# Optimization experiments

Hardware: AMD Instinct MI355X
Metric: run time of the kernel (lower is better)

The kernel has to match this reference:

```python
import jax, jax.numpy as jnp
import numpy as np

N, E, F, H, C, K = 50000, 1600000, 256, 6, 16, 40
NEG_SLOPE = 0.2  # PyG GATConv default
EPS = 1e-16


def _gat_layer(x, src, dst, W, a_s, a_d, b, heads, out_ch, concat):
    # linear transform per head: [N, heads, out_ch]
    h = (x @ W).reshape(N, heads, out_ch)
    # per-node attention logits
    al_s = jnp.einsum('nhc,hc->nh', h, a_s)  # source term
    al_d = jnp.einsum('nhc,hc->nh', h, a_d)  # destination term
    # edge-wise score + segment softmax over incoming edges of each dst node
    e = jax.nn.leaky_relu(al_s[src] + al_d[dst], NEG_SLOPE)  # [E', heads]
    m = jax.ops.segment_max(e, dst, num_segments=N)
    ex = jnp.exp(e - m[dst])
    denom = jax.ops.segment_sum(ex, dst, num_segments=N)
    alpha = ex / (denom[dst] + EPS)  # [E', heads]
    # weighted scatter-add aggregation
    out = jax.ops.segment_sum(h[src] * alpha[:, :, None], dst, num_segments=N)
    out = out.reshape(N, heads * out_ch) if concat else out.mean(axis=1)
    return out + b


def setup_inputs() -> dict:
    key = jax.random.key(0)
    ks = jax.random.split(key, 16)
    s = 0.05
    inp = {
        'x': jax.random.normal(ks[0], (N, F), dtype=jnp.float32),
        'edge_index': jax.random.randint(ks[1], (2, E), 0, N, dtype=jnp.int64 if jax.config.jax_enable_x64 else jnp.int32),
        'W1': jax.random.normal(ks[2], (F, H * C), dtype=jnp.float32) * s,
        'a1_s': jax.random.normal(ks[3], (H, C), dtype=jnp.float32) * s,
        'a1_d': jax.random.normal(ks[4], (H, C), dtype=jnp.float32) * s,
        'b1': jnp.zeros((H * C,), dtype=jnp.float32),
        'W2': jax.random.normal(ks[5], (H * C, H * C), dtype=jnp.float32) * s,
        'a2_s': jax.random.normal(ks[6], (H, C), dtype=jnp.float32) * s,
        'a2_d': jax.random.normal(ks[7], (H, C), dtype=jnp.float32) * s,
        'b2': jnp.zeros((H * C,), dtype=jnp.float32),
        'W3': jax.random.normal(ks[8], (H * C, H * C), dtype=jnp.float32) * s,
        'a3_s': jax.random.normal(ks[9], (H, C), dtype=jnp.float32) * s,
        'a3_d': jax.random.normal(ks[10], (H, C), dtype=jnp.float32) * s,
        'b3': jnp.zeros((H * C,), dtype=jnp.float32),
        'W4': jax.random.normal(ks[11], (H * C, K), dtype=jnp.float32) * s,
        'a4_s': jax.random.normal(ks[12], (1, K), dtype=jnp.float32) * s,
        'a4_d': jax.random.normal(ks[13], (1, K), dtype=jnp.float32) * s,
        'b4': jnp.zeros((K,), dtype=jnp.float32),
    }
    return inp


def reference(x, edge_index, W1, a1_s, a1_d, b1, W2, a2_s, a2_d, b2,
              W3, a3_s, a3_d, b3, W4, a4_s, a4_d, b4):
    # PyG GATConv adds self-loops by default
    loops = jnp.arange(N, dtype=edge_index.dtype)
    src = jnp.concatenate([edge_index[0], loops])
    dst = jnp.concatenate([edge_index[1], loops])
    # dropout is identity at eval time
    h = jax.nn.relu(_gat_layer(x, src, dst, W1, a1_s, a1_d, b1, H, C, True))
    h = jax.nn.relu(_gat_layer(h, src, dst, W2, a2_s, a2_d, b2, H, C, True))
    h = jax.nn.relu(_gat_layer(h, src, dst, W3, a3_s, a3_d, b3, H, C, True))
    h = _gat_layer(h, src, dst, W4, a4_s, a4_d, b4, 1, K, False)
    return jax.nn.log_softmax(h, axis=1)
```

## Files before the change

### kernel.cpp

```cpp
#include <hip/hip_runtime.h>
#include <cstdint>
#include <cstddef>

namespace {

constexpr int N  = 50000;
constexpr int E  = 1600000;
constexpr int ET = E + N;
constexpr int F  = 256;
constexpr int H  = 6;
constexpr int C  = 16;
constexpr int HC = H * C;
constexpr int K  = 40;
constexpr int NBUCK = (N + 255) / 256;
constexpr int EPB2  = 8192;
constexpr int HBLK  = (ET + EPB2 - 1) / EPB2;

typedef __attribute__((ext_vector_type(8))) short short8;
typedef __attribute__((ext_vector_type(4))) float f32x4;
typedef __attribute__((ext_vector_type(2))) float f32x2;

__device__ inline uint32_t f2bf(float f) {
  uint32_t u = __float_as_uint(f);
  return (u + 0x7FFFu + ((u >> 16) & 1u)) >> 16;
}
__device__ inline float bflo(uint32_t u) { return __uint_as_float(u << 16); }
__device__ inline float bfhi(uint32_t u) { return __uint_as_float(u & 0xFFFF0000u); }


__global__ void coarse_hist_kernel(const int* __restrict__ ei, int* __restrict__ hist) {
  __shared__ int h[256];
  const int t = threadIdx.x;
  h[t] = 0;
  __syncthreads();
  const int cbase = blockIdx.x * EPB2;
  const int cend = (cbase + EPB2 < ET) ? (cbase + EPB2) : ET;
  for (int e0 = cbase + t * 4; e0 < cend; e0 += 1024) {
    if (e0 + 3 < E && e0 + 3 < cend) {
      int4 dv = *reinterpret_cast<const int4*>(ei + E + e0);
      atomicAdd(&h[dv.x >> 8], 1);
      atomicAdd(&h[dv.y >> 8], 1);
      atomicAdd(&h[dv.z >> 8], 1);
      atomicAdd(&h[dv.w >> 8], 1);
    } else {
#pragma unroll
      for (int q = 0; q < 4; q++) {
        int e = e0 + q;
        if (e < cend) {
          int dd = (e < E) ? ei[E + e] : (e - E);
          atomicAdd(&h[dd >> 8], 1);
        }
      }
    }
  }
  __syncthreads();
  hist[blockIdx.x * 256 + t] = h[t];
}

__global__ void coarse_scan_kernel(const int* __restrict__ hist, int* __restrict__ base,
                                   int* __restrict__ bucket_base, int* __restrict__ rowp) {
  __shared__ int sc[256];
  const int d = threadIdx.x;
  int tot = 0;
#pragma unroll 4
  for (int b = 0; b < HBLK; b++) tot += hist[b * 256 + d];
  sc[d] = tot;
  __syncthreads();
  for (int off = 1; off < 256; off <<= 1) {
    int tv = (d >= off) ? sc[d - off] : 0;
    __syncthreads();
    sc[d] += tv;
    __syncthreads();
  }
  const int excl = sc[d] - tot;
  bucket_base[d] = excl;
  if (d == 255) {
    bucket_base[256] = sc[255];
    rowp[N] = sc[255];
  }
  int run = excl;
#pragma unroll 4
  for (int b = 0; b < HBLK; b++) {
    int v = hist[b * 256 + d];
    base[b * 256 + d] = run;
    run += v;
  }
}

__global__ void coarse_scatter_kernel(const int* __restrict__ ei, const int* __restrict__ base,
                                      uint32_t* __restrict__ keys) {
  __shared__ int cnt[256];
  const int t = threadIdx.x;
  cnt[t] = base[blockIdx.x * 256 + t];
  __syncthreads();
  const int cbase = blockIdx.x * EPB2;
  const int cend = (cbase + EPB2 < ET) ? (cbase + EPB2) : ET;
  for (int e0 = cbase + t * 4; e0 < cend; e0 += 1024) {
    if (e0 + 3 < E && e0 + 3 < cend) {
      int4 dv = *reinterpret_cast<const int4*>(ei + E + e0);
      int4 sv = *reinterpret_cast<const int4*>(ei + e0);
      int p0 = atomicAdd(&cnt[dv.x >> 8], 1);
      keys[p0] = ((uint32_t)dv.x << 16) | (uint32_t)sv.x;
      int p1 = atomicAdd(&cnt[dv.y >> 8], 1);
      keys[p1] = ((uint32_t)dv.y << 16) | (uint32_t)sv.y;
      int p2 = atomicAdd(&cnt[dv.z >> 8], 1);
      keys[p2] = ((uint32_t)dv.z << 16) | (uint32_t)sv.z;
      int p3 = atomicAdd(&cnt[dv.w >> 8], 1);
      keys[p3] = ((uint32_t)dv.w << 16) | (uint32_t)sv.w;
    } else {
#pragma unroll
      for (int q = 0; q < 4; q++) {
        int e = e0 + q;
        if (e < cend) {
          int dd, ssrc;
          if (e < E) { dd = ei[E + e]; ssrc = ei[e]; }
          else       { dd = e - E; ssrc = e - E; }
          int p = atomicAdd(&cnt[dd >> 8], 1);
          keys[p] = ((uint32_t)dd << 16) | (uint32_t)ssrc;
        }
      }
    }
  }
}

__global__ void bucket_sort_kernel(const uint32_t* __restrict__ keys,
                                   const int* __restrict__ bucket_base,
                                   int* __restrict__ rowp, int* __restrict__ col) {
  __shared__ int hist[256];
  __shared__ int sc[256];
  __shared__ int ofs[256];
  const int b = blockIdx.x;
  const int t = threadIdx.x;
  hist[t] = 0;
  __syncthreads();
  const int k0 = bucket_base[b], k1 = bucket_base[b + 1];
  for (int i = k0 + t; i < k1; i += 256)
    atomicAdd(&hist[(keys[i] >> 16) & 255], 1);
  __syncthreads();
  const int v = hist[t];
  sc[t] = v;
  __syncthreads();
  for (int off = 1; off < 256; off <<= 1) {
    int tv = (t >= off) ? sc[t - off] : 0;
    __syncthreads();
    sc[t] += tv;
    __syncthreads();
  }
  ofs[t] = k0 + sc[t] - v;
  const int node = b * 256 + t;
  if (node < N) rowp[node] = ofs[t];
  hist[t] = 0;
  __syncthreads();
  for (int i = k0 + t; i < k1; i += 256) {
    uint32_t key = keys[i];
    int loc = (key >> 16) & 255;
    int p = ofs[loc] + atomicAdd(&hist[loc], 1);
    col[p] = (int)(key & 0xFFFFu);
  }
}


__global__ void deg_hist_kernel(const int* __restrict__ rowp, int* __restrict__ dh) {
  __shared__ int h[256];
  const int t = threadIdx.x;
  h[t] = 0;
  __syncthreads();
  int i = blockIdx.x * 256 + t;
  if (i < N) {
    int deg = rowp[i + 1] - rowp[i];
    if (deg > 255) deg = 255;
    atomicAdd(&h[deg], 1);
  }
  __syncthreads();
  dh[blockIdx.x * 256 + t] = h[t];
}

__global__ void deg_scan_kernel(const int* __restrict__ dh, int* __restrict__ dbase) {
  __shared__ int sc[256];
  const int d = threadIdx.x;
  int tot = 0;
#pragma unroll 4
  for (int b = 0; b < NBUCK; b++) tot += dh[b * 256 + d];
  sc[d] = tot;
  __syncthreads();
  for (int off = 1; off < 256; off <<= 1) {
    int tv = (d >= off) ? sc[d - off] : 0;
    __syncthreads();
    sc[d] += tv;
    __syncthreads();
  }
  int run = sc[d] - tot;
#pragma unroll 4
  for (int b = 0; b < NBUCK; b++) {
    int v = dh[b * 256 + d];
    dbase[b * 256 + d] = run;
    run += v;
  }
}

__global__ void deg_scatter_kernel(const int* __restrict__ rowp, const int* __restrict__ dbase,
                                   int* __restrict__ perm) {
  __shared__ int cnt[256];
  const int t = threadIdx.x;
  cnt[t] = dbase[blockIdx.x * 256 + t];
  __syncthreads();
  int i = blockIdx.x * 256 + t;
  if (i < N) {
    int deg = rowp[i + 1] - rowp[i];
    if (deg > 255) deg = 255;
    int p = atomicAdd(&cnt[deg], 1);
    perm[p] = i;
  }
}


__global__ void tobf16_kernel(const float* __restrict__ src, uint32_t* __restrict__ dst,
                              int n2) {
  int i = blockIdx.x * blockDim.x + threadIdx.x;
  if (i >= n2) return;
  float2 v = reinterpret_cast<const float2*>(src)[i];
  dst[i] = (f2bf(v.y) << 16) | f2bf(v.x);
}


__global__ void cvtW_kernel(const float* __restrict__ W1, const float* __restrict__ W2,
                            const float* __restrict__ W3, const float* __restrict__ W4,
                            uint16_t* __restrict__ WT1, uint16_t* __restrict__ WT2,
                            uint16_t* __restrict__ WT3, uint16_t* __restrict__ WT4) {
  constexpr int T1 = 96 * 256, T2 = 96 * 96, T3 = 96 * 96, T4 = 48 * 96;
  int t = blockIdx.x * blockDim.x + threadIdx.x;
  if (t < T1) {
    int n = t / 256, k = t % 256;
    WT1[t] = (uint16_t)f2bf(W1[(size_t)k * 96 + n]);
  } else if (t < T1 + T2) {
    int u = t - T1; int n = u / 96, k = u % 96;
    WT2[u] = (uint16_t)f2bf(W2[(size_t)k * 96 + n]);
  } else if (t < T1 + T2 + T3) {
    int u = t - T1 - T2; int n = u / 96, k = u % 96;
    WT3[u] = (uint16_t)f2bf(W3[(size_t)k * 96 + n]);
  } else if (t < T1 + T2 + T3 + T4) {
    int u = t - T1 - T2 - T3; int n = u / 96, k = u % 96;
    WT4[u] = (n < K) ? (uint16_t)f2bf(W4[(size_t)k * K + n]) : (uint16_t)0;
  }
}


template <int KD>
__launch_bounds__(256)
__global__ void gemm_pack_kernel(const uint32_t* __restrict__ A,
                                 const uint16_t* __restrict__ WT,
                                 const float* __restrict__ as_,
                                 const float* __restrict__ ad_,
                                 uint32_t* __restrict__ recs,
                                 float* __restrict__ aldP) {
  constexpr int KU = KD / 2;
  __shared__ float lds[64][97];
  const int wave = threadIdx.x >> 6;
  const int lane = threadIdx.x & 63;
  const int r = lane & 15, g = lane >> 4;
  const int m0 = (blockIdx.x * 4 + wave) * 16;
  int rowA = m0 + r;
  if (rowA > N - 1) rowA = N - 1;
  const uint32_t* arow = A + (size_t)rowA * KU + g * 4;
  const uint32_t* wt32 = reinterpret_cast<const uint32_t*>(WT);

  f32x4 acc[6];
#pragma unroll
  for (int nt = 0; nt < 6; nt++) acc[nt] = (f32x4){0.f, 0.f, 0.f, 0.f};

#pragma unroll
  for (int ks = 0; ks < KD / 32; ks++) {
    short8 av = *reinterpret_cast<const short8*>(arow + ks * 16);
#pragma unroll
    for (int nt = 0; nt < 6; nt++) {
      short8 bv = *reinterpret_cast<const short8*>(
          wt32 + (size_t)(nt * 16 + r) * KU + ks * 16 + g * 4);
      acc[nt] = __builtin_amdgcn_mfma_f32_16x16x32_bf16(av, bv, acc[nt], 0, 0, 0);
    }
  }

  const int lr0 = wave * 16 + g * 4;
#pragma unroll
  for (int nt = 0; nt < 6; nt++) {
#pragma unroll
    for (int t = 0; t < 4; t++) lds[lr0 + t][nt * 16 + r] = acc[nt][t];
  }
  __syncthreads();

  const int row = threadIdx.x >> 2;
  const int q = threadIdx.x & 3;
  const int grow = blockIdx.x * 64 + row;
  if (grow < N) {
    const float* lr = lds[row];
    uint32_t* rp = recs + (size_t)grow * 32;
#pragma unroll
    for (int w = 0; w < 6; w++) {
      const int c0 = q * 24 + w * 4;
      uint32_t wv = 0;
      wv = (uint32_t)__builtin_amdgcn_cvt_pk_fp8_f32(lr[c0], lr[c0 + 1], (int)wv, false);
      wv = (uint32_t)__builtin_amdgcn_cvt_pk_fp8_f32(lr[c0 + 2], lr[c0 + 3], (int)wv, true);
      rp[q * 6 + w] = wv;
    }
#pragma unroll
    for (int i = 0; i < 3; i++) {
      const int d = q * 3 + i;
      const int hh = d >> 1;
      const float* av = (d & 1) ? ad_ : as_;
      float s = 0.f;
#pragma unroll
      for (int c = 0; c < 16; c++) s += lr[hh * 16 + c] * av[hh * 16 + c];
      if (d & 1) aldP[(size_t)grow * 8 + hh] = s;
      else       rp[24 + hh] = __float_as_uint(s);
    }
  }
}


template <int KD, int NT, int NCOLS, int OST>
__launch_bounds__(256)
__global__ void mfma_gemm_kernel(const uint32_t* __restrict__ A,
                                 const uint16_t* __restrict__ WT,
                                 uint16_t* __restrict__ hOut, int M) {
  constexpr int KU = KD / 2;
  const int wave = threadIdx.x >> 6;
  const int lane = threadIdx.x & 63;
  const int m0 = (blockIdx.x * 4 + wave) * 16;
  if (m0 >= M) return;
  const int r = lane & 15, g = lane >> 4;
  int rowA = m0 + r;
  if (rowA > M - 1) rowA = M - 1;
  const uint32_t* arow = A + (size_t)rowA * KU + g * 4;
  const uint32_t* wt32 = reinterpret_cast<const uint32_t*>(WT);

  f32x4 acc[NT];
#pragma unroll
  for (int nt = 0; nt < NT; nt++) acc[nt] = (f32x4){0.f, 0.f, 0.f, 0.f};

#pragma unroll
  for (int ks = 0; ks < KD / 32; ks++) {
    short8 av = *reinterpret_cast<const short8*>(arow + ks * 16);
#pragma unroll
    for (int nt = 0; nt < NT; nt++) {
      short8 bv = *reinterpret_cast<const short8*>(
          wt32 + (size_t)(nt * 16 + r) * KU + ks * 16 + g * 4);
      acc[nt] = __builtin_amdgcn_mfma_f32_16x16x32_bf16(av, bv, acc[nt], 0, 0, 0);
    }
  }

  const int orow = m0 + g * 4;
#pragma unroll
  for (int nt = 0; nt < NT; nt++) {
    const int ocol = nt * 16 + r;
#pragma unroll
    for (int t = 0; t < 4; t++) {
      int rr = orow + t;
      if (rr < M && ocol < NCOLS)
        hOut[(size_t)rr * OST + ocol] = (uint16_t)f2bf(acc[nt][t]);
    }
  }
}


__global__ void pack4_kernel(const uint32_t* __restrict__ h4B,
                             const float* __restrict__ as_, const float* __restrict__ ad_,
                             uint32_t* __restrict__ recs4, float* __restrict__ ald4) {
  int n = blockIdx.x * 256 + threadIdx.x;
  if (n >= N) return;
  const uint32_t* hp = h4B + (size_t)n * 32;
  float f[40];
  float ss = 0.f, dd = 0.f;
#pragma unroll
  for (int i = 0; i < 20; i++) {
    uint32_t u = hp[i];
    f[2 * i] = bflo(u);
    f[2 * i + 1] = bfhi(u);
  }
#pragma unroll
  for (int c = 0; c < 40; c++) {
    ss += f[c] * as_[c];
    dd += f[c] * ad_[c];
  }
  uint32_t* rp = recs4 + (size_t)n * 16;
#pragma unroll
  for (int q = 0; q < 10; q++) {
    uint32_t w = 0;
    w = (uint32_t)__builtin_amdgcn_cvt_pk_fp8_f32(f[4 * q + 0], f[4 * q + 1], (int)w, false);
    w = (uint32_t)__builtin_amdgcn_cvt_pk_fp8_f32(f[4 * q + 2], f[4 * q + 3], (int)w, true);
    rp[q] = w;
  }
  rp[10] = __float_as_uint(ss);
  ald4[n] = dd;
}


template <int LPN, int NPW, int REC32, int ALSW, int HDIV, int PAD, bool LSM>
__launch_bounds__(256)
__global__ void flash_agg5_kernel(const uint32_t* __restrict__ recs,
                                  const int* __restrict__ rowp,
                                  const int* __restrict__ col,
                                  const int* __restrict__ perm,
                                  const float* __restrict__ aldP,
                                  const float* __restrict__ bias,
                                  uint4* __restrict__ outB4,
                                  float* __restrict__ outF32) {
  const int lane = threadIdx.x & 63;
  const int wave = threadIdx.x >> 6;
  int g = lane / LPN;
  const int li = lane - g * LPN;
  if (g > NPW - 1) g = NPW - 1;
  int idx = (blockIdx.x * 4 + wave) * NPW + g;
  if (idx > N - 1) idx = N - 1;
  const int n = perm[idx];
  const int hh = li / HDIV;
  const float aldv = aldP[(size_t)n * PAD + hh];
  const int b0 = rowp[n];
  const int deg = rowp[n + 1] - b0;
  const int d1 = deg >> 1;
  const int d2 = deg - d1;

  int km = d2;
#pragma unroll
  for (int off = 32; off > 0; off >>= 1) {
    int o = __shfl_xor(km, off);
    km = (o > km) ? o : km;
  }

  float a0 = 0.f, a1 = 0.f, a2 = 0.f, a3 = 0.f;
  float a4 = 0.f, a5 = 0.f, a6 = 0.f, a7 = 0.f;
  float b0f = 0.f, b1f = 0.f, b2f = 0.f, b3f = 0.f;
  float b4f = 0.f, b5f = 0.f, b6f = 0.f, b7f = 0.f;
  float ssA = 0.f, ssB = 0.f;

#pragma unroll 2
  for (int k = 0; k < km; k++) {
    const bool vA = (k < d1);
    const bool vB = (k < d2);
    const int jA = b0 + (vA ? k : 0);
    const int jB = b0 + d1 + (vB ? k : 0);
    const int srcA = col[jA];
    const int srcB = col[jB];
    const uint32_t* recA = recs + (size_t)srcA * REC32;
    const uint32_t* recB = recs + (size_t)srcB * REC32;
    uint2 uA = *reinterpret_cast<const uint2*>(recA + 2 * li);
    uint2 uB = *reinterpret_cast<const uint2*>(recB + 2 * li);
    float lA = __uint_as_float(recA[ALSW + hh]);
    float lB = __uint_as_float(recB[ALSW + hh]);
    float eA = lA + aldv; eA = fmaxf(eA, 0.2f * eA);
    float eB = lB + aldv; eB = fmaxf(eB, 0.2f * eB);
    float pA = __expf(eA); pA = vA ? pA : 0.f;
    float pB = __expf(eB); pB = vB ? pB : 0.f;
    f32x2 cA0 = __builtin_amdgcn_cvt_pk_f32_fp8((int)uA.x, false);
    f32x2 cA1 = __builtin_amdgcn_cvt_pk_f32_fp8((int)uA.x, true);
    f32x2 cA2 = __builtin_amdgcn_cvt_pk_f32_fp8((int)uA.y, false);
    f32x2 cA3 = __builtin_amdgcn_cvt_pk_f32_fp8((int)uA.y, true);
    f32x2 cB0 = __builtin_amdgcn_cvt_pk_f32_fp8((int)uB.x, false);
    f32x2 cB1 = __builtin_amdgcn_cvt_pk_f32_fp8((int)uB.x, true);
    f32x2 cB2 = __builtin_amdgcn_cvt_pk_f32_fp8((int)uB.y, false);
    f32x2 cB3 = __builtin_amdgcn_cvt_pk_f32_fp8((int)uB.y, true);
    a0 += pA * cA0.x; a1 += pA * cA0.y;
    a2 += pA * cA1.x; a3 += pA * cA1.y;
    a4 += pA * cA2.x; a5 += pA * cA2.y;
    a6 += pA * cA3.x; a7 += pA * cA3.y;
    ssA += pA;
    b0f += pB * cB0.x; b1f += pB * cB0.y;
    b2f += pB * cB1.x; b3f += pB * cB1.y;
    b4f += pB * cB2.x; b5f += pB * cB2.y;
    b6f += pB * cB3.x; b7f += pB * cB3.y;
    ssB += pB;
  }

  a0 += b0f; a1 += b1f; a2 += b2f; a3 += b3f;
  a4 += b4f; a5 += b5f; a6 += b6f; a7 += b7f;
  float inv = 1.f / (ssA + ssB + 1e-16f);

  if (!LSM) {
    float o0 = fmaxf(a0 * inv + bias[8 * li + 0], 0.f);
    float o1 = fmaxf(a1 * inv + bias[8 * li + 1], 0.f);
    float o2 = fmaxf(a2 * inv + bias[8 * li + 2], 0.f);
    float o3 = fmaxf(a3 * inv + bias[8 * li + 3], 0.f);
    float o4 = fmaxf(a4 * inv + bias[8 * li + 4], 0.f);
    float o5 = fmaxf(a5 * inv + bias[8 * li + 5], 0.f);
    float o6 = fmaxf(a6 * inv + bias[8 * li + 6], 0.f);
    float o7 = fmaxf(a7 * inv + bias[8 * li + 7], 0.f);
    uint4 w;
    w.x = (f2bf(o1) << 16) | f2bf(o0);
    w.y = (f2bf(o3) << 16) | f2bf(o2);
    w.z = (f2bf(o5) << 16) | f2bf(o4);
    w.w = (f2bf(o7) << 16) | f2bf(o6);
    outB4[(size_t)n * LPN + li] = w;
  } else {
    bool vl = (li < 5);
    float v0 = vl ? a0 * inv + bias[8 * li + 0] : -1e30f;
    float v1 = vl ? a1 * inv + bias[8 * li + 1] : -1e30f;
    float v2 = vl ? a2 * inv + bias[8 * li + 2] : -1e30f;
    float v3 = vl ? a3 * inv + bias[8 * li + 3] : -1e30f;
    float v4 = vl ? a4 * inv + bias[8 * li + 4] : -1e30f;
    float v5 = vl ? a5 * inv + bias[8 * li + 5] : -1e30f;
    float v6 = vl ? a6 * inv + bias[8 * li + 6] : -1e30f;
    float v7 = vl ? a7 * inv + bias[8 * li + 7] : -1e30f;
    float mx = fmaxf(fmaxf(fmaxf(v0, v1), fmaxf(v2, v3)),
                     fmaxf(fmaxf(v4, v5), fmaxf(v6, v7)));
#pragma unroll
    for (int off = 1; off < 8; off <<= 1) mx = fmaxf(mx, __shfl_xor(mx, off));
    float es = 0.f;
    if (vl)
      es = __expf(v0 - mx) + __expf(v1 - mx) + __expf(v2 - mx) + __expf(v3 - mx) +
           __expf(v4 - mx) + __expf(v5 - mx) + __expf(v6 - mx) + __expf(v7 - mx);
#pragma unroll
    for (int off = 1; off < 8; off <<= 1) es += __shfl_xor(es, off);
    float lse = mx + __logf(es);
    if (vl) {
      float* op = outF32 + (size_t)n * K + li * 8;
      float4 w0 = make_float4(v0 - lse, v1 - lse, v2 - lse, v3 - lse);
      float4 w1 = make_float4(v4 - lse, v5 - lse, v6 - lse, v7 - lse);
      *reinterpret_cast<float4*>(op) = w0;
      *reinterpret_cast<float4*>(op + 4) = w1;
    }
  }
}

inline int cdiv(int a, int b) { return (a + b - 1) / b; }

}

extern "C" void kernel_launch(void* const* d_in, const int* in_sizes, int n_in,
                              void* d_out, int out_size, void* d_ws, size_t ws_size,
                              hipStream_t stream) {
  (void)in_sizes; (void)n_in; (void)out_size; (void)ws_size;
  const float* x   = (const float*)d_in[0];
  const int*   ei  = (const int*)d_in[1];
  const float* W1  = (const float*)d_in[2];
  const float* a1s = (const float*)d_in[3];
  const float* a1d = (const float*)d_in[4];
  const float* b1  = (const float*)d_in[5];
  const float* W2  = (const float*)d_in[6];
  const float* a2s = (const float*)d_in[7];
  const float* a2d = (const float*)d_in[8];
  const float* b2  = (const float*)d_in[9];
  const float* W3  = (const float*)d_in[10];
  const float* a3s = (const float*)d_in[11];
  const float* a3d = (const float*)d_in[12];
  const float* b3  = (const float*)d_in[13];
  const float* W4  = (const float*)d_in[14];
  const float* a4s = (const float*)d_in[15];
  const float* a4d = (const float*)d_in[16];
  const float* b4  = (const float*)d_in[17];
  float* out = (float*)d_out;

  char* ws = (char*)d_ws;
  size_t off = 0;
  auto alloc = [&](size_t bytes) {
    void* p = ws + off;
    off = (off + bytes + 255) & ~(size_t)255;
    return p;
  };
  int*      hist  = (int*)alloc((size_t)HBLK * 256 * 4);
  int*      basep = (int*)alloc((size_t)HBLK * 256 * 4);
  int*      bbase = (int*)alloc((size_t)257 * 4);
  int*      rowp  = (int*)alloc((size_t)(N + 1) * 4);
  uint32_t* keys  = (uint32_t*)alloc((size_t)ET * 4);
  int*      col   = (int*)alloc((size_t)ET * 4);
  int*      perm  = (int*)alloc((size_t)N * 4);
  uint32_t* xB    = (uint32_t*)alloc((size_t)N * (F / 2) * 4);
  uint16_t* WT1   = (uint16_t*)alloc((size_t)96 * 256 * 2);
  uint16_t* WT2   = (uint16_t*)alloc((size_t)96 * 96 * 2);
  uint16_t* WT3   = (uint16_t*)alloc((size_t)96 * 96 * 2);
  uint16_t* WT4   = (uint16_t*)alloc((size_t)48 * 96 * 2);
  uint32_t* actB  = (uint32_t*)alloc((size_t)N * (HC / 2) * 4);
  uint32_t* h4B   = (uint32_t*)alloc((size_t)N * 32 * 4);
  uint32_t* recs  = (uint32_t*)alloc((size_t)N * 32 * 4);
  uint32_t* recs4 = (uint32_t*)alloc((size_t)N * 16 * 4);
  float*    aldP  = (float*)alloc((size_t)N * 8 * 4);

  coarse_hist_kernel<<<HBLK, 256, 0, stream>>>(ei, hist);
  coarse_scan_kernel<<<1, 256, 0, stream>>>(hist, basep, bbase, rowp);
  coarse_scatter_kernel<<<HBLK, 256, 0, stream>>>(ei, basep, keys);
  bucket_sort_kernel<<<NBUCK, 256, 0, stream>>>(keys, bbase, rowp, col);

  deg_hist_kernel<<<NBUCK, 256, 0, stream>>>(rowp, hist);
  deg_scan_kernel<<<1, 256, 0, stream>>>(hist, basep);
  deg_scatter_kernel<<<NBUCK, 256, 0, stream>>>(rowp, basep, perm);

  tobf16_kernel<<<cdiv(N * (F / 2), 256), 256, 0, stream>>>(x, xB, N * (F / 2));
  cvtW_kernel<<<cdiv(96 * 256 + 96 * 96 * 2 + 48 * 96, 256), 256, 0, stream>>>(
      W1, W2, W3, W4, WT1, WT2, WT3, WT4);

  const int gN1  = cdiv(N, 256);
  const int gG   = cdiv(N, 64);
  const int gA96 = cdiv(N, 20);
  const int gA40 = cdiv(N, 32);

  gemm_pack_kernel<F><<<gG, 256, 0, stream>>>(xB, WT1, a1s, a1d, recs, aldP);
  flash_agg5_kernel<12, 5, 32, 24, 2, 8, false><<<gA96, 256, 0, stream>>>(
      recs, rowp, col, perm, aldP, b1, (uint4*)actB, nullptr);

  gemm_pack_kernel<HC><<<gG, 256, 0, stream>>>(actB, WT2, a2s, a2d, recs, aldP);
  flash_agg5_kernel<12, 5, 32, 24, 2, 8, false><<<gA96, 256, 0, stream>>>(
      recs, rowp, col, perm, aldP, b2, (uint4*)actB, nullptr);

  gemm_pack_kernel<HC><<<gG, 256, 0, stream>>>(actB, WT3, a3s, a3d, recs, aldP);
  flash_agg5_kernel<12, 5, 32, 24, 2, 8, false><<<gA96, 256, 0, stream>>>(
      recs, rowp, col, perm, aldP, b3, (uint4*)actB, nullptr);

  mfma_gemm_kernel<HC, 3, K, 64><<<gG, 256, 0, stream>>>(actB, WT4, (uint16_t*)h4B, N);
  pack4_kernel<<<gN1, 256, 0, stream>>>(h4B, a4s, a4d, recs4, aldP);
  flash_agg5_kernel<8, 8, 16, 10, 16, 1, true><<<gA40, 256, 0, stream>>>(
      recs4, rowp, col, perm, aldP, b4, nullptr, out);
}
```

Before: 309.3 us.

## Map one lane per head in hidden-layer aggregation, 10 nodes per wave

Hidden-layer aggregation now assigns 6 lanes per destination node, one per head, each loading 16 fp8 features with a uint4 instead of 12 lanes each loading 8. A wave now handles 10 nodes instead of 5, which halves the grid and lowers redundant col/logit loads per edge. The price is more accumulator registers per lane and 4 idle lanes per wave. Separately, the x and weight bf16 conversion kernels are merged into one launch, and the layer-4 log-softmax path becomes its own kernel.

```diff
diff --git a/kernel.cpp b/kernel.cpp
--- a/kernel.cpp
+++ b/kernel.cpp
@@ -214,21 +214,22 @@
 }
 
 
-__global__ void tobf16_kernel(const float* __restrict__ src, uint32_t* __restrict__ dst,
-                              int n2) {
-  int i = blockIdx.x * blockDim.x + threadIdx.x;
-  if (i >= n2) return;
-  float2 v = reinterpret_cast<const float2*>(src)[i];
-  dst[i] = (f2bf(v.y) << 16) | f2bf(v.x);
-}
-
-
-__global__ void cvtW_kernel(const float* __restrict__ W1, const float* __restrict__ W2,
+constexpr int TOB_N2 = N * (F / 2);
+constexpr int T1 = 96 * 256, T2 = 96 * 96, T3 = 96 * 96, T4 = 48 * 96;
+constexpr int CVT_T = T1 + T2 + T3 + T4;
+
+__global__ void prep_kernel(const float* __restrict__ x, uint32_t* __restrict__ xB,
+                            const float* __restrict__ W1, const float* __restrict__ W2,
                             const float* __restrict__ W3, const float* __restrict__ W4,
                             uint16_t* __restrict__ WT1, uint16_t* __restrict__ WT2,
                             uint16_t* __restrict__ WT3, uint16_t* __restrict__ WT4) {
-  constexpr int T1 = 96 * 256, T2 = 96 * 96, T3 = 96 * 96, T4 = 48 * 96;
-  int t = blockIdx.x * blockDim.x + threadIdx.x;
+  int t = blockIdx.x * 256 + threadIdx.x;
+  if (t < TOB_N2) {
+    float2 v = reinterpret_cast<const float2*>(x)[t];
+    xB[t] = (f2bf(v.y) << 16) | f2bf(v.x);
+    return;
+  }
+  t -= TOB_N2;
   if (t < T1) {
     int n = t / 256, k = t % 256;
     WT1[t] = (uint16_t)f2bf(W1[(size_t)k * 96 + n]);
@@ -238,7 +239,7 @@
   } else if (t < T1 + T2 + T3) {
     int u = t - T1 - T2; int n = u / 96, k = u % 96;
     WT3[u] = (uint16_t)f2bf(W3[(size_t)k * 96 + n]);
-  } else if (t < T1 + T2 + T3 + T4) {
+  } else if (t < CVT_T) {
     int u = t - T1 - T2 - T3; int n = u / 96, k = u % 96;
     WT4[u] = (n < K) ? (uint16_t)f2bf(W4[(size_t)k * K + n]) : (uint16_t)0;
   }
@@ -393,26 +394,24 @@
 }
 
 
-template <int LPN, int NPW, int REC32, int ALSW, int HDIV, int PAD, bool LSM>
 __launch_bounds__(256)
-__global__ void flash_agg5_kernel(const uint32_t* __restrict__ recs,
+__global__ void flash_agg6_kernel(const uint32_t* __restrict__ recs,
                                   const int* __restrict__ rowp,
                                   const int* __restrict__ col,
                                   const int* __restrict__ perm,
                                   const float* __restrict__ aldP,
                                   const float* __restrict__ bias,
-                                  uint4* __restrict__ outB4,
-                                  float* __restrict__ outF32) {
+                                  uint4* __restrict__ outB4) {
   const int lane = threadIdx.x & 63;
   const int wave = threadIdx.x >> 6;
-  int g = lane / LPN;
-  const int li = lane - g * LPN;
-  if (g > NPW - 1) g = NPW - 1;
-  int idx = (blockIdx.x * 4 + wave) * NPW + g;
+  int g = lane / 6;
+  if (g > 9) g = 9;
+  int li = lane - g * 6;
+  if (li > 5) li = 5;
+  int idx = (blockIdx.x * 4 + wave) * 10 + g;
   if (idx > N - 1) idx = N - 1;
   const int n = perm[idx];
-  const int hh = li / HDIV;
-  const float aldv = aldP[(size_t)n * PAD + hh];
+  const float aldv = aldP[(size_t)n * 8 + li];
   const int b0 = rowp[n];
   const int deg = rowp[n + 1] - b0;
   const int d1 = deg >> 1;
@@ -425,10 +424,9 @@
     km = (o > km) ? o : km;
   }
 
-  float a0 = 0.f, a1 = 0.f, a2 = 0.f, a3 = 0.f;
-  float a4 = 0.f, a5 = 0.f, a6 = 0.f, a7 = 0.f;
-  float b0f = 0.f, b1f = 0.f, b2f = 0.f, b3f = 0.f;
-  float b4f = 0.f, b5f = 0.f, b6f = 0.f, b7f = 0.f;
+  float accA[16], accB[16];
+#pragma unroll
+  for (int c = 0; c < 16; c++) { accA[c] = 0.f; accB[c] = 0.f; }
   float ssA = 0.f, ssB = 0.f;
 
 #pragma unroll 2
@@ -439,12 +437,93 @@
     const int jB = b0 + d1 + (vB ? k : 0);
     const int srcA = col[jA];
     const int srcB = col[jB];
-    const uint32_t* recA = recs + (size_t)srcA * REC32;
-    const uint32_t* recB = recs + (size_t)srcB * REC32;
+    const uint32_t* recA = recs + (size_t)srcA * 32;
+    const uint32_t* recB = recs + (size_t)srcB * 32;
+    uint4 uA = *reinterpret_cast<const uint4*>(recA + 4 * li);
+    uint4 uB = *reinterpret_cast<const uint4*>(recB + 4 * li);
+    float lA = __uint_as_float(recA[24 + li]);
+    float lB = __uint_as_float(recB[24 + li]);
+    float eA = lA + aldv; eA = fmaxf(eA, 0.2f * eA);
+    float eB = lB + aldv; eB = fmaxf(eB, 0.2f * eB);
+    float pA = __expf(eA); pA = vA ? pA : 0.f;
+    float pB = __expf(eB); pB = vB ? pB : 0.f;
+    const uint32_t wa[4] = {uA.x, uA.y, uA.z, uA.w};
+    const uint32_t wb[4] = {uB.x, uB.y, uB.z, uB.w};
+#pragma unroll
+    for (int w = 0; w < 4; w++) {
+      f32x2 c0 = __builtin_amdgcn_cvt_pk_f32_fp8((int)wa[w], false);
+      f32x2 c1 = __builtin_amdgcn_cvt_pk_f32_fp8((int)wa[w], true);
+      accA[4 * w + 0] += pA * c0.x; accA[4 * w + 1] += pA * c0.y;
+      accA[4 * w + 2] += pA * c1.x; accA[4 * w + 3] += pA * c1.y;
+      f32x2 d0 = __builtin_amdgcn_cvt_pk_f32_fp8((int)wb[w], false);
+      f32x2 dd1 = __builtin_amdgcn_cvt_pk_f32_fp8((int)wb[w], true);
+      accB[4 * w + 0] += pB * d0.x; accB[4 * w + 1] += pB * d0.y;
+      accB[4 * w + 2] += pB * dd1.x; accB[4 * w + 3] += pB * dd1.y;
+    }
+    ssA += pA; ssB += pB;
+  }
+
+  const float inv = 1.f / (ssA + ssB + 1e-16f);
+  uint32_t wout[8];
+#pragma unroll
+  for (int j = 0; j < 8; j++) {
+    float o0 = fmaxf((accA[2 * j] + accB[2 * j]) * inv + bias[16 * li + 2 * j], 0.f);
+    float o1 = fmaxf((accA[2 * j + 1] + accB[2 * j + 1]) * inv + bias[16 * li + 2 * j + 1], 0.f);
+    wout[j] = (f2bf(o1) << 16) | f2bf(o0);
+  }
+  outB4[(size_t)n * 12 + 2 * li]     = make_uint4(wout[0], wout[1], wout[2], wout[3]);
+  outB4[(size_t)n * 12 + 2 * li + 1] = make_uint4(wout[4], wout[5], wout[6], wout[7]);
+}
+
+
+__launch_bounds__(256)
+__global__ void flash_agg_lsm_kernel(const uint32_t* __restrict__ recs,
+                                     const int* __restrict__ rowp,
+                                     const int* __restrict__ col,
+                                     const int* __restrict__ perm,
+                                     const float* __restrict__ aldP,
+                                     const float* __restrict__ bias,
+                                     float* __restrict__ outF32) {
+  const int lane = threadIdx.x & 63;
+  const int wave = threadIdx.x >> 6;
+  const int g = lane >> 3;
+  const int li = lane & 7;
+  int idx = (blockIdx.x * 4 + wave) * 8 + g;
+  if (idx > N - 1) idx = N - 1;
+  const int n = perm[idx];
+  const float aldv = aldP[n];
+  const int b0 = rowp[n];
+  const int deg = rowp[n + 1] - b0;
+  const int d1 = deg >> 1;
+  const int d2 = deg - d1;
+
+  int km = d2;
+#pragma unroll
+  for (int off = 32; off > 0; off >>= 1) {
+    int o = __shfl_xor(km, off);
+    km = (o > km) ? o : km;
+  }
+
+  float a0 = 0.f, a1 = 0.f, a2 = 0.f, a3 = 0.f;
+  float a4 = 0.f, a5 = 0.f, a6 = 0.f, a7 = 0.f;
+  float b0f = 0.f, b1f = 0.f, b2f = 0.f, b3f = 0.f;
+  float b4f = 0.f, b5f = 0.f, b6f = 0.f, b7f = 0.f;
+  float ssA = 0.f, ssB = 0.f;
+
+#pragma unroll 2
+  for (int k = 0; k < km; k++) {
+    const bool vA = (k < d1);
+    const bool vB = (k < d2);
+    const int jA = b0 + (vA ? k : 0);
+    const int jB = b0 + d1 + (vB ? k : 0);
+    const int srcA = col[jA];
+    const int srcB = col[jB];
+    const uint32_t* recA = recs + (size_t)srcA * 16;
+    const uint32_t* recB = recs + (size_t)srcB * 16;
     uint2 uA = *reinterpret_cast<const uint2*>(recA + 2 * li);
     uint2 uB = *reinterpret_cast<const uint2*>(recB + 2 * li);
-    float lA = __uint_as_float(recA[ALSW + hh]);
-    float lB = __uint_as_float(recB[ALSW + hh]);
+    float lA = __uint_as_float(recA[10]);
+    float lB = __uint_as_float(recB[10]);
     float eA = lA + aldv; eA = fmaxf(eA, 0.2f * eA);
     float eB = lB + aldv; eB = fmaxf(eB, 0.2f * eB);
     float pA = __expf(eA); pA = vA ? pA : 0.f;
@@ -473,49 +552,30 @@
   a4 += b4f; a5 += b5f; a6 += b6f; a7 += b7f;
   float inv = 1.f / (ssA + ssB + 1e-16f);
 
-  if (!LSM) {
-    float o0 = fmaxf(a0 * inv + bias[8 * li + 0], 0.f);
-    float o1 = fmaxf(a1 * inv + bias[8 * li + 1], 0.f);
-    float o2 = fmaxf(a2 * inv + bias[8 * li + 2], 0.f);
-    float o3 = fmaxf(a3 * inv + bias[8 * li + 3], 0.f);
-    float o4 = fmaxf(a4 * inv + bias[8 * li + 4], 0.f);
-    float o5 = fmaxf(a5 * inv + bias[8 * li + 5], 0.f);
-    float o6 = fmaxf(a6 * inv + bias[8 * li + 6], 0.f);
-    float o7 = fmaxf(a7 * inv + bias[8 * li + 7], 0.f);
-    uint4 w;
-    w.x = (f2bf(o1) << 16) | f2bf(o0);
-    w.y = (f2bf(o3) << 16) | f2bf(o2);
-    w.z = (f2bf(o5) << 16) | f2bf(o4);
-    w.w = (f2bf(o7) << 16) | f2bf(o6);
-    outB4[(size_t)n * LPN + li] = w;
-  } else {
-    bool vl = (li < 5);
-    float v0 = vl ? a0 * inv + bias[8 * li + 0] : -1e30f;
-    float v1 = vl ? a1 * inv + bias[8 * li + 1] : -1e30f;
-    float v2 = vl ? a2 * inv + bias[8 * li + 2] : -1e30f;
-    float v3 = vl ? a3 * inv + bias[8 * li + 3] : -1e30f;
-    float v4 = vl ? a4 * inv + bias[8 * li + 4] : -1e30f;
-    float v5 = vl ? a5 * inv + bias[8 * li + 5] : -1e30f;
-    float v6 = vl ? a6 * inv + bias[8 * li + 6] : -1e30f;
-    float v7 = vl ? a7 * inv + bias[8 * li + 7] : -1e30f;
-    float mx = fmaxf(fmaxf(fmaxf(v0, v1), fmaxf(v2, v3)),
-                     fmaxf(fmaxf(v4, v5), fmaxf(v6, v7)));
-#pragma unroll
-    for (int off = 1; off < 8; off <<= 1) mx = fmaxf(mx, __shfl_xor(mx, off));
-    float es = 0.f;
-    if (vl)
-      es = __expf(v0 - mx) + __expf(v1 - mx) + __expf(v2 - mx) + __expf(v3 - mx) +
-           __expf(v4 - mx) + __expf(v5 - mx) + __expf(v6 - mx) + __expf(v7 - mx);
-#pragma unroll
-    for (int off = 1; off < 8; off <<= 1) es += __shfl_xor(es, off);
-    float lse = mx + __logf(es);
-    if (vl) {
-      float* op = outF32 + (size_t)n * K + li * 8;
-      float4 w0 = make_float4(v0 - lse, v1 - lse, v2 - lse, v3 - lse);
-      float4 w1 = make_float4(v4 - lse, v5 - lse, v6 - lse, v7 - lse);
-      *reinterpret_cast<float4*>(op) = w0;
-      *reinterpret_cast<float4*>(op + 4) = w1;
-    }
+  bool vl = (li < 5);
+  float v0 = vl ? a0 * inv + bias[8 * li + 0] : -1e30f;
+  float v1 = vl ? a1 * inv + bias[8 * li + 1] : -1e30f;
+  float v2 = vl ? a2 * inv + bias[8 * li + 2] : -1e30f;
+  float v3 = vl ? a3 * inv + bias[8 * li + 3] : -1e30f;
+  float v4 = vl ? a4 * inv + bias[8 * li + 4] : -1e30f;
+  float v5 = vl ? a5 * inv + bias[8 * li + 5] : -1e30f;
+  float v6 = vl ? a6 * inv + bias[8 * li + 6] : -1e30f;
+  float v7 = vl ? a7 * inv + bias[8 * li + 7] : -1e30f;
+  float mx = fmaxf(fmaxf(fmaxf(v0, v1), fmaxf(v2, v3)),
+                   fmaxf(fmaxf(v4, v5), fmaxf(v6, v7)));
+#pragma unroll
+  for (int off = 1; off < 8; off <<= 1) mx = fmaxf(mx, __shfl_xor(mx, off));
+  float es = 0.f;
+  if (vl)
+    es = __expf(v0 - mx) + __expf(v1 - mx) + __expf(v2 - mx) + __expf(v3 - mx) +
+         __expf(v4 - mx) + __expf(v5 - mx) + __expf(v6 - mx) + __expf(v7 - mx);
+#pragma unroll
+  for (int off = 1; off < 8; off <<= 1) es += __shfl_xor(es, off);
+  float lse = mx + __logf(es);
+  if (vl) {
+    float* op = outF32 + (size_t)n * K + li * 8;
+    *reinterpret_cast<float4*>(op) = make_float4(v0 - lse, v1 - lse, v2 - lse, v3 - lse);
+    *reinterpret_cast<float4*>(op + 4) = make_float4(v4 - lse, v5 - lse, v6 - lse, v7 - lse);
   }
 }
 
@@ -581,29 +641,24 @@
   deg_scan_kernel<<<1, 256, 0, stream>>>(hist, basep);
   deg_scatter_kernel<<<NBUCK, 256, 0, stream>>>(rowp, basep, perm);
 
-  tobf16_kernel<<<cdiv(N * (F / 2), 256), 256, 0, stream>>>(x, xB, N * (F / 2));
-  cvtW_kernel<<<cdiv(96 * 256 + 96 * 96 * 2 + 48 * 96, 256), 256, 0, stream>>>(
-      W1, W2, W3, W4, WT1, WT2, WT3, WT4);
+  prep_kernel<<<cdiv(TOB_N2 + CVT_T, 256), 256, 0, stream>>>(
+      x, xB, W1, W2, W3, W4, WT1, WT2, WT3, WT4);
 
   const int gN1  = cdiv(N, 256);
   const int gG   = cdiv(N, 64);
-  const int gA96 = cdiv(N, 20);
+  const int gA96 = cdiv(N, 40);
   const int gA40 = cdiv(N, 32);
 
   gemm_pack_kernel<F><<<gG, 256, 0, stream>>>(xB, WT1, a1s, a1d, recs, aldP);
-  flash_agg5_kernel<12, 5, 32, 24, 2, 8, false><<<gA96, 256, 0, stream>>>(
-      recs, rowp, col, perm, aldP, b1, (uint4*)actB, nullptr);
+  flash_agg6_kernel<<<gA96, 256, 0, stream>>>(recs, rowp, col, perm, aldP, b1, (uint4*)actB);
 
   gemm_pack_kernel<HC><<<gG, 256, 0, stream>>>(actB, WT2, a2s, a2d, recs, aldP);
-  flash_agg5_kernel<12, 5, 32, 24, 2, 8, false><<<gA96, 256, 0, stream>>>(
-      recs, rowp, col, perm, aldP, b2, (uint4*)actB, nullptr);
+  flash_agg6_kernel<<<gA96, 256, 0, stream>>>(recs, rowp, col, perm, aldP, b2, (uint4*)actB);
 
   gemm_pack_kernel<HC><<<gG, 256, 0, stream>>>(actB, WT3, a3s, a3d, recs, aldP);
-  flash_agg5_kernel<12, 5, 32, 24, 2, 8, false><<<gA96, 256, 0, stream>>>(
-      recs, rowp, col, perm, aldP, b3, (uint4*)actB, nullptr);
+  flash_agg6_kernel<<<gA96, 256, 0, stream>>>(recs, rowp, col, perm, aldP, b3, (uint4*)actB);
 
   mfma_gemm_kernel<HC, 3, K, 64><<<gG, 256, 0, stream>>>(actB, WT4, (uint16_t*)h4B, N);
   pack4_kernel<<<gN1, 256, 0, stream>>>(h4B, a4s, a4d, recs4, aldP);
-  flash_agg5_kernel<8, 8, 16, 10, 16, 1, true><<<gA40, 256, 0, stream>>>(
-      recs4, rowp, col, perm, aldP, b4, nullptr, out);
-}
+  flash_agg_lsm_kernel<<<gA40, 256, 0, stream>>>(recs4, rowp, col, perm, aldP, b4, out);
+}
```

Result: slower. 317.6 us (+2.7%).

## Fuse input/weight conversion, fuse layer-4 GEMM with packing, reverse degree order

Applied to the files above, without the earlier changes.

Merges the x-to-bf16 conversion and weight transpose kernels into a single prep kernel. Fuses the final-layer MFMA GEMM with the fp8 record packing and attention logit computation through LDS, removing the intermediate bf16 h4 buffer and one launch. Reverses the degree-sorted node permutation so high-degree nodes are scheduled first, aiming to reduce tail imbalance in aggregation. The fused pack step runs on only one wave per block, which serializes some per-row work.

```diff
diff --git a/kernel.cpp b/kernel.cpp
--- a/kernel.cpp
+++ b/kernel.cpp
@@ -209,26 +209,27 @@
     int deg = rowp[i + 1] - rowp[i];
     if (deg > 255) deg = 255;
     int p = atomicAdd(&cnt[deg], 1);
-    perm[p] = i;
-  }
-}
-
-
-__global__ void tobf16_kernel(const float* __restrict__ src, uint32_t* __restrict__ dst,
-                              int n2) {
-  int i = blockIdx.x * blockDim.x + threadIdx.x;
-  if (i >= n2) return;
-  float2 v = reinterpret_cast<const float2*>(src)[i];
-  dst[i] = (f2bf(v.y) << 16) | f2bf(v.x);
-}
-
-
-__global__ void cvtW_kernel(const float* __restrict__ W1, const float* __restrict__ W2,
+    perm[N - 1 - p] = i;
+  }
+}
+
+
+constexpr int TOB_N2 = N * (F / 2);
+constexpr int T1 = 96 * 256, T2 = 96 * 96, T3 = 96 * 96, T4 = 48 * 96;
+constexpr int CVT_T = T1 + T2 + T3 + T4;
+
+__global__ void prep_kernel(const float* __restrict__ x, uint32_t* __restrict__ xB,
+                            const float* __restrict__ W1, const float* __restrict__ W2,
                             const float* __restrict__ W3, const float* __restrict__ W4,
                             uint16_t* __restrict__ WT1, uint16_t* __restrict__ WT2,
                             uint16_t* __restrict__ WT3, uint16_t* __restrict__ WT4) {
-  constexpr int T1 = 96 * 256, T2 = 96 * 96, T3 = 96 * 96, T4 = 48 * 96;
-  int t = blockIdx.x * blockDim.x + threadIdx.x;
+  int t = blockIdx.x * 256 + threadIdx.x;
+  if (t < TOB_N2) {
+    float2 v = reinterpret_cast<const float2*>(x)[t];
+    xB[t] = (f2bf(v.y) << 16) | f2bf(v.x);
+    return;
+  }
+  t -= TOB_N2;
   if (t < T1) {
     int n = t / 256, k = t % 256;
     WT1[t] = (uint16_t)f2bf(W1[(size_t)k * 96 + n]);
@@ -238,7 +239,7 @@
   } else if (t < T1 + T2 + T3) {
     int u = t - T1 - T2; int n = u / 96, k = u % 96;
     WT3[u] = (uint16_t)f2bf(W3[(size_t)k * 96 + n]);
-  } else if (t < T1 + T2 + T3 + T4) {
+  } else if (t < CVT_T) {
     int u = t - T1 - T2 - T3; int n = u / 96, k = u % 96;
     WT4[u] = (n < K) ? (uint16_t)f2bf(W4[(size_t)k * K + n]) : (uint16_t)0;
   }
@@ -316,80 +317,70 @@
 }
 
 
-template <int KD, int NT, int NCOLS, int OST>
 __launch_bounds__(256)
-__global__ void mfma_gemm_kernel(const uint32_t* __restrict__ A,
-                                 const uint16_t* __restrict__ WT,
-                                 uint16_t* __restrict__ hOut, int M) {
-  constexpr int KU = KD / 2;
+__global__ void gemm_pack4_kernel(const uint32_t* __restrict__ A,
+                                  const uint16_t* __restrict__ WT,
+                                  const float* __restrict__ as_,
+                                  const float* __restrict__ ad_,
+                                  uint32_t* __restrict__ recs4,
+                                  float* __restrict__ ald4) {
+  constexpr int KU = 48;
+  __shared__ float lds[64][49];
   const int wave = threadIdx.x >> 6;
   const int lane = threadIdx.x & 63;
+  const int r = lane & 15, g = lane >> 4;
   const int m0 = (blockIdx.x * 4 + wave) * 16;
-  if (m0 >= M) return;
-  const int r = lane & 15, g = lane >> 4;
   int rowA = m0 + r;
-  if (rowA > M - 1) rowA = M - 1;
+  if (rowA > N - 1) rowA = N - 1;
   const uint32_t* arow = A + (size_t)rowA * KU + g * 4;
   const uint32_t* wt32 = reinterpret_cast<const uint32_t*>(WT);
 
-  f32x4 acc[NT];
-#pragma unroll
-  for (int nt = 0; nt < NT; nt++) acc[nt] = (f32x4){0.f, 0.f, 0.f, 0.f};
-
-#pragma unroll
-  for (int ks = 0; ks < KD / 32; ks++) {
+  f32x4 acc[3];
+#pragma unroll
+  for (int nt = 0; nt < 3; nt++) acc[nt] = (f32x4){0.f, 0.f, 0.f, 0.f};
+
+#pragma unroll
+  for (int ks = 0; ks < 3; ks++) {
     short8 av = *reinterpret_cast<const short8*>(arow + ks * 16);
 #pragma unroll
-    for (int nt = 0; nt < NT; nt++) {
+    for (int nt = 0; nt < 3; nt++) {
       short8 bv = *reinterpret_cast<const short8*>(
           wt32 + (size_t)(nt * 16 + r) * KU + ks * 16 + g * 4);
       acc[nt] = __builtin_amdgcn_mfma_f32_16x16x32_bf16(av, bv, acc[nt], 0, 0, 0);
     }
   }
 
-  const int orow = m0 + g * 4;
-#pragma unroll
-  for (int nt = 0; nt < NT; nt++) {
-    const int ocol = nt * 16 + r;
-#pragma unroll
-    for (int t = 0; t < 4; t++) {
-      int rr = orow + t;
-      if (rr < M && ocol < NCOLS)
-        hOut[(size_t)rr * OST + ocol] = (uint16_t)f2bf(acc[nt][t]);
-    }
-  }
-}
-
-
-__global__ void pack4_kernel(const uint32_t* __restrict__ h4B,
-                             const float* __restrict__ as_, const float* __restrict__ ad_,
-                             uint32_t* __restrict__ recs4, float* __restrict__ ald4) {
-  int n = blockIdx.x * 256 + threadIdx.x;
-  if (n >= N) return;
-  const uint32_t* hp = h4B + (size_t)n * 32;
-  float f[40];
-  float ss = 0.f, dd = 0.f;
-#pragma unroll
-  for (int i = 0; i < 20; i++) {
-    uint32_t u = hp[i];
-    f[2 * i] = bflo(u);
-    f[2 * i + 1] = bfhi(u);
-  }
-#pragma unroll
-  for (int c = 0; c < 40; c++) {
-    ss += f[c] * as_[c];
-    dd += f[c] * ad_[c];
-  }
-  uint32_t* rp = recs4 + (size_t)n * 16;
-#pragma unroll
-  for (int q = 0; q < 10; q++) {
-    uint32_t w = 0;
-    w = (uint32_t)__builtin_amdgcn_cvt_pk_fp8_f32(f[4 * q + 0], f[4 * q + 1], (int)w, false);
-    w = (uint32_t)__builtin_amdgcn_cvt_pk_fp8_f32(f[4 * q + 2], f[4 * q + 3], (int)w, true);
-    rp[q] = w;
-  }
-  rp[10] = __float_as_uint(ss);
-  ald4[n] = dd;
+  const int lr0 = wave * 16 + g * 4;
+#pragma unroll
+  for (int nt = 0; nt < 3; nt++) {
+#pragma unroll
+    for (int t = 0; t < 4; t++) lds[lr0 + t][nt * 16 + r] = acc[nt][t];
+  }
+  __syncthreads();
+
+  if (threadIdx.x < 64) {
+    const int row = threadIdx.x;
+    const int grow = blockIdx.x * 64 + row;
+    if (grow < N) {
+      const float* lr = lds[row];
+      float ss = 0.f, dd = 0.f;
+#pragma unroll
+      for (int c = 0; c < 40; c++) {
+        ss += lr[c] * as_[c];
+        dd += lr[c] * ad_[c];
+      }
+      uint32_t* rp = recs4 + (size_t)grow * 16;
+#pragma unroll
+      for (int q = 0; q < 10; q++) {
+        uint32_t w = 0;
+        w = (uint32_t)__builtin_amdgcn_cvt_pk_fp8_f32(lr[4 * q], lr[4 * q + 1], (int)w, false);
+        w = (uint32_t)__builtin_amdgcn_cvt_pk_fp8_f32(lr[4 * q + 2], lr[4 * q + 3], (int)w, true);
+        rp[q] = w;
+      }
+      rp[10] = __float_as_uint(ss);
+      ald4[grow] = dd;
+    }
+  }
 }
 
 
@@ -567,7 +558,6 @@
   uint16_t* WT3   = (uint16_t*)alloc((size_t)96 * 96 * 2);
   uint16_t* WT4   = (uint16_t*)alloc((size_t)48 * 96 * 2);
   uint32_t* actB  = (uint32_t*)alloc((size_t)N * (HC / 2) * 4);
-  uint32_t* h4B   = (uint32_t*)alloc((size_t)N * 32 * 4);
   uint32_t* recs  = (uint32_t*)alloc((size_t)N * 32 * 4);
   uint32_t* recs4 = (uint32_t*)alloc((size_t)N * 16 * 4);
   float*    aldP  = (float*)alloc((size_t)N * 8 * 4);
@@ -581,11 +571,9 @@
   deg_scan_kernel<<<1, 256, 0, stream>>>(hist, basep);
   deg_scatter_kernel<<<NBUCK, 256, 0, stream>>>(rowp, basep, perm);
 
-  tobf16_kernel<<<cdiv(N * (F / 2), 256), 256, 0, stream>>>(x, xB, N * (F / 2));
-  cvtW_kernel<<<cdiv(96 * 256 + 96 * 96 * 2 + 48 * 96, 256), 256, 0, stream>>>(
-      W1, W2, W3, W4, WT1, WT2, WT3, WT4);
-
-  const int gN1  = cdiv(N, 256);
+  prep_kernel<<<cdiv(TOB_N2 + CVT_T, 256), 256, 0, stream>>>(
+      x, xB, W1, W2, W3, W4, WT1, WT2, WT3, WT4);
+
   const int gG   = cdiv(N, 64);
   const int gA96 = cdiv(N, 20);
   const int gA40 = cdiv(N, 32);
@@ -602,8 +590,7 @@
   flash_agg5_kernel<12, 5, 32, 24, 2, 8, false><<<gA96, 256, 0, stream>>>(
       recs, rowp, col, perm, aldP, b3, (uint4*)actB, nullptr);
 
-  mfma_gemm_kernel<HC, 3, K, 64><<<gG, 256, 0, stream>>>(actB, WT4, (uint16_t*)h4B, N);
-  pack4_kernel<<<gN1, 256, 0, stream>>>(h4B, a4s, a4d, recs4, aldP);
+  gemm_pack4_kernel<<<gG, 256, 0, stream>>>(actB, WT4, a4s, a4d, recs4, aldP);
   flash_agg5_kernel<8, 8, 16, 10, 16, 1, true><<<gA40, 256, 0, stream>>>(
       recs4, rowp, col, perm, aldP, b4, nullptr, out);
 }
```

Result: faster. 289.4 us (-6.4%).
